# Performance work log

Measured on AMD Instinct MI355X. Metric: run time of the kernel, lower is better.

Reference implementation:

```python
import jax, jax.numpy as jnp
import numpy as np

NEG_SLOPE = 0.2  # PyG GATConv leaky_relu negative_slope
EPS = 1e-16      # PyG softmax denominator epsilon


def _add_self_loops(edge_index, edge_attr, N):
    # PyG add_self_loops with fill_value='mean': loop attr = mean of incoming edge attrs
    src, dst = edge_index[0], edge_index[1]
    ones = jnp.ones((src.shape[0],), edge_attr.dtype)
    cnt = jax.ops.segment_sum(ones, dst, num_segments=N)
    loop_attr = jax.ops.segment_sum(edge_attr, dst, num_segments=N) / jnp.maximum(cnt, 1.0)[:, None]
    loops = jnp.arange(N, dtype=src.dtype)
    return (jnp.concatenate([src, loops]),
            jnp.concatenate([dst, loops]),
            jnp.concatenate([edge_attr, loop_attr], axis=0))


def _gat_conv(x, src, dst, ea, W, We, att_src, att_dst, att_edge, bias, heads, out_ch):
    N = x.shape[0]
    h = (x @ W).reshape(N, heads, out_ch)              # [N,H,C]
    a_src = (h * att_src).sum(-1)                      # [N,H]
    a_dst = (h * att_dst).sum(-1)                      # [N,H]
    e = (ea @ We).reshape(-1, heads, out_ch)           # [E,H,C]
    a_edge = (e * att_edge).sum(-1)                    # [E,H]
    alpha = jax.nn.leaky_relu(a_src[src] + a_dst[dst] + a_edge, NEG_SLOPE)
    amax = jax.ops.segment_max(alpha, dst, num_segments=N)
    alpha = jnp.exp(alpha - amax[dst])
    denom = jax.ops.segment_sum(alpha, dst, num_segments=N)
    alpha = alpha / (denom[dst] + EPS)
    out = jax.ops.segment_sum(h[src] * alpha[..., None], dst, num_segments=N)  # [N,H,C]
    return out.mean(axis=1) + bias                     # concat=False -> mean over heads


def setup_inputs() -> dict:
    key = jax.random.key(0)
    ks = jax.random.split(key, 16)
    N, E, F_in, HID, OUT, H = 50000, 800000, 64, 16, 8, 8
    s = 0.1
    return {
        "x": jax.random.normal(ks[0], (N, F_in), jnp.float32),
        "edge_index": jax.random.randint(ks[1], (2, E), 0, N, dtype=jnp.int64),
        "edge_attr": jax.random.uniform(ks[2], (E, 1), jnp.float32),
        "W1": jax.random.normal(ks[3], (F_in, H * HID), jnp.float32) * s,
        "We1": jax.random.normal(ks[4], (1, H * HID), jnp.float32) * s,
        "att_src1": jax.random.normal(ks[5], (H, HID), jnp.float32) * s,
        "att_dst1": jax.random.normal(ks[6], (H, HID), jnp.float32) * s,
        "att_edge1": jax.random.normal(ks[7], (H, HID), jnp.float32) * s,
        "b1": jnp.zeros((HID,), jnp.float32),
        "W2": jax.random.normal(ks[8], (HID, OUT), jnp.float32) * s,
        "We2": jax.random.normal(ks[9], (1, OUT), jnp.float32) * s,
        "att_src2": jax.random.normal(ks[10], (1, OUT), jnp.float32) * s,
        "att_dst2": jax.random.normal(ks[11], (1, OUT), jnp.float32) * s,
        "att_edge2": jax.random.normal(ks[12], (1, OUT), jnp.float32) * s,
        "b2": jnp.zeros((OUT,), jnp.float32),
    }


def reference(x, edge_index, edge_attr, W1, We1, att_src1, att_dst1, att_edge1, b1,
              W2, We2, att_src2, att_dst2, att_edge2, b2):
    N = x.shape[0]
    src, dst, ea = _add_self_loops(edge_index, edge_attr, N)
    h = jax.nn.relu(_gat_conv(x, src, dst, ea, W1, We1, att_src1, att_dst1, att_edge1, b1, 8, 16))
    # dropout is identity in eval mode
    return _gat_conv(h, src, dst, ea, W2, We2, att_src2, att_dst2, att_edge2, b2, 1, 8)
```

## Files before the change

kernel.cpp:

```cpp
#include <hip/hip_runtime.h>
#include <hip/hip_fp16.h>
#include <math.h>

#define EPS 1e-16f
#define LOG2E 1.44269504088896340736f

typedef _Float16 half8 __attribute__((ext_vector_type(8)));
typedef float floatx4 __attribute__((ext_vector_type(4)));

#define RNG 4
#define NRR 16384
#define RB  64


__global__ __launch_bounds__(256) void k_hist(int E, int CH, const int* __restrict__ ei,
                                              int* __restrict__ H, int* __restrict__ rank) {
    int r = blockIdx.x / RB, b = blockIdx.x % RB;
    __shared__ int hist[NRR];
    for (int i = threadIdx.x; i < NRR; i += 256) hist[i] = 0;
    __syncthreads();
    int lo = b * CH, hi = min(E, (b + 1) * CH);
    int rlo = r << 14;
#pragma unroll 4
    for (int e = lo + threadIdx.x; e < hi; e += 256) {
        int d = ei[E + e];
        int dr = d - rlo;
        if ((unsigned)dr < NRR) rank[e] = atomicAdd(&hist[dr], 1);
    }
    __syncthreads();
    int* Hb = H + (size_t)blockIdx.x * NRR;
    for (int i = threadIdx.x; i < NRR; i += 256) Hb[i] = hist[i];
}

__global__ __launch_bounds__(256) void k_cntscan(int N, int* __restrict__ H,
                                                 int* rowptr, int* bsums) {
    __shared__ int sm[256];
    int t = threadIdx.x;
    int n = blockIdx.x * 256 + t;
    int sum = 0;
    if (n < N) {
        int r = n >> 14, dr = n & (NRR - 1);
        size_t base = ((size_t)(r * RB)) * NRR + dr;
#pragma unroll 8
        for (int b = 0; b < RB; ++b) {
            size_t idx = base + (size_t)b * NRR;
            int v = H[idx];
            H[idx] = sum;
            sum += v;
        }
    }
    int val = (n < N) ? (sum + 1) : 0;
    sm[t] = val; __syncthreads();
    for (int ofs = 1; ofs < 256; ofs <<= 1) {
        int v = (t >= ofs) ? sm[t - ofs] : 0;
        __syncthreads();
        sm[t] += v;
        __syncthreads();
    }
    if (n < N) rowptr[n] = sm[t] - val;
    if (t == 255) bsums[blockIdx.x] = sm[255];
}

__global__ void k_scan2(int nb, int N, int* bsums, int* rowptr) {
    __shared__ int sm[256];
    int t = threadIdx.x;
    int v = (t < nb) ? bsums[t] : 0;
    sm[t] = v; __syncthreads();
    for (int ofs = 1; ofs < 256; ofs <<= 1) {
        int u = (t >= ofs) ? sm[t - ofs] : 0;
        __syncthreads();
        sm[t] += u;
        __syncthreads();
    }
    if (t < nb) bsums[t] = sm[t] - v;
    if (t == 255) rowptr[N] = sm[255];
}

__global__ void k_scan3(int N, int* rowptr, const int* __restrict__ bsums) {
    int n = blockIdx.x * blockDim.x + threadIdx.x;
    if (n < N) rowptr[n] += bsums[n >> 8];
}

__global__ void k_scatter(int E, int CH, const int* __restrict__ ei, const float* __restrict__ ea,
                          const int* __restrict__ rowptr, const int* __restrict__ H,
                          const int* __restrict__ rank, int2* __restrict__ rec) {
    int e = blockIdx.x * blockDim.x + threadIdx.x;
    if (e >= E) return;
    int s = ei[e], d = ei[E + e];
    int r = d >> 14, dr = d & (NRR - 1);
    int b = e / CH;
    int pos = rowptr[d] + H[((size_t)(r * RB + b)) * NRR + dr] + rank[e];
    unsigned long long pk = ((unsigned long long)(unsigned)__float_as_int(ea[e]) << 32)
                          | (unsigned long long)(unsigned)s;
    __builtin_nontemporal_store(pk, (unsigned long long*)&rec[pos]);
}


__global__ __launch_bounds__(256) void k_misc(
    int N, int nbN, int Mpad, const int* __restrict__ rowptr, int2* __restrict__ rec,
    const float* __restrict__ x, _Float16* __restrict__ xh,
    const float* __restrict__ W1, _Float16* __restrict__ Wpk,
    const float* __restrict__ We1, const float* __restrict__ ae1,
    const float* __restrict__ We2, const float* __restrict__ ae2,
    float* __restrict__ wed) {
    int bid = blockIdx.x;
    if (bid < nbN) {
        int d = bid * 256 + threadIdx.x;
        if (d < N) {
            int start = rowptr[d], slot = rowptr[d + 1] - 1;
            float ssum = 0.0f;
            for (int i = start; i < slot; ++i) ssum += __int_as_float(rec[i].y);
            float mean = ssum / fmaxf((float)(slot - start), 1.0f);
            rec[slot] = make_int2(d, __float_as_int(mean));
        }
    } else if (bid < nbN + Mpad / 32) {
        int t = (bid - nbN) * 256 + threadIdx.x;
        int row = t >> 3;
        half8 h;
        if (row < N) {
            const float4* pp = (const float4*)(x + (size_t)t * 8);
            float4 f0 = pp[0], f1 = pp[1];
            h[0] = (_Float16)f0.x; h[1] = (_Float16)f0.y; h[2] = (_Float16)f0.z; h[3] = (_Float16)f0.w;
            h[4] = (_Float16)f1.x; h[5] = (_Float16)f1.y; h[6] = (_Float16)f1.z; h[7] = (_Float16)f1.w;
        } else {
#pragma unroll
            for (int i = 0; i < 8; ++i) h[i] = (_Float16)0.0f;
        }
        *(half8*)(xh + (size_t)t * 8) = h;
    } else {
        int t = threadIdx.x;
        for (int i = 0; i < 32; ++i) {
            int idx = i * 256 + t;
            int j  = idx & 7;
            int lq = (idx >> 3) & 63;
            int ks = (idx >> 9) & 1;
            int ct = idx >> 10;
            int k   = ks * 32 + (lq >> 4) * 8 + j;
            int col = ct * 16 + (lq & 15);
            Wpk[idx] = (_Float16)W1[k * 128 + col];
        }
        if (t < 8) {
            float ssum = 0.0f;
            for (int cc = 0; cc < 16; ++cc) ssum += We1[t * 16 + cc] * ae1[t * 16 + cc];
            wed[t] = ssum * LOG2E;
        }
        if (t == 8) {
            float ssum = 0.0f;
            for (int cc = 0; cc < 8; ++cc) ssum += We2[cc] * ae2[cc];
            wed[8] = ssum * LOG2E;
        }
    }
}


#define LDSP 132

__global__ __launch_bounds__(256) void k_gemm1m(
    int N, const _Float16* __restrict__ xh, const _Float16* __restrict__ Wpk,
    const float* __restrict__ att_s, const float* __restrict__ att_d,
    __half* __restrict__ h1, float* __restrict__ asrc, float* __restrict__ adst) {
    __shared__ float hs[4 * 16 * LDSP];
    int tid = threadIdx.x;
    int w = tid >> 6, l = tid & 63;
    int row0 = blockIdx.x * 64 + w * 16;
    int arow = row0 + (l & 15);
    half8 a0 = *(const half8*)(xh + (size_t)arow * 64 + (l >> 4) * 8);
    half8 a1 = *(const half8*)(xh + (size_t)arow * 64 + 32 + (l >> 4) * 8);
    float* base = &hs[w * 16 * LDSP];
    int r0 = (l >> 4) * 4;
#pragma unroll
    for (int ct = 0; ct < 8; ++ct) {
        half8 b0 = *(const half8*)(Wpk + ((ct * 2 + 0) * 64 + l) * 8);
        half8 b1 = *(const half8*)(Wpk + ((ct * 2 + 1) * 64 + l) * 8);
        floatx4 acc = {0.f, 0.f, 0.f, 0.f};
        acc = __builtin_amdgcn_mfma_f32_16x16x32_f16(a0, b0, acc, 0, 0, 0);
        acc = __builtin_amdgcn_mfma_f32_16x16x32_f16(a1, b1, acc, 0, 0, 0);
        int col = ct * 16 + (l & 15);
#pragma unroll
        for (int i = 0; i < 4; ++i)
            base[(r0 + i) * LDSP + col] = acc[i];
    }
    __syncthreads();
    int r = tid >> 2, g = tid & 3;
    int rg = blockIdx.x * 64 + r;
    if (rg >= N) return;
    float v[32];
    const float* rp = &hs[r * LDSP + g * 32];
#pragma unroll
    for (int j = 0; j < 8; ++j) {
        floatx4 t4 = *(const floatx4*)(rp + j * 4);
        v[j * 4 + 0] = t4[0]; v[j * 4 + 1] = t4[1];
        v[j * 4 + 2] = t4[2]; v[j * 4 + 3] = t4[3];
    }
    float vs0 = 0.f, vs1 = 0.f, vd0 = 0.f, vd1 = 0.f;
    const float4* as4 = (const float4*)(att_s + g * 32);
    const float4* ad4 = (const float4*)(att_d + g * 32);
#pragma unroll
    for (int j = 0; j < 4; ++j) {
        float4 a4 = as4[j], d4 = ad4[j];
        vs0 += v[j*4+0]*a4.x + v[j*4+1]*a4.y + v[j*4+2]*a4.z + v[j*4+3]*a4.w;
        vd0 += v[j*4+0]*d4.x + v[j*4+1]*d4.y + v[j*4+2]*d4.z + v[j*4+3]*d4.w;
    }
#pragma unroll
    for (int j = 4; j < 8; ++j) {
        float4 a4 = as4[j], d4 = ad4[j];
        vs1 += v[j*4+0]*a4.x + v[j*4+1]*a4.y + v[j*4+2]*a4.z + v[j*4+3]*a4.w;
        vd1 += v[j*4+0]*d4.x + v[j*4+1]*d4.y + v[j*4+2]*d4.z + v[j*4+3]*d4.w;
    }
    union { __half h[32]; float4 f4[4]; } u;
#pragma unroll
    for (int i = 0; i < 32; ++i) u.h[i] = __float2half(v[i]);
    float4* hp = (float4*)(h1 + (size_t)rg * 128 + g * 32);
#pragma unroll
    for (int j = 0; j < 4; ++j) hp[j] = u.f4[j];
    asrc[rg * 8 + g * 2]     = vs0 * LOG2E;
    asrc[rg * 8 + g * 2 + 1] = vs1 * LOG2E;
    adst[rg * 8 + g * 2]     = vd0 * LOG2E;
    adst[rg * 8 + g * 2 + 1] = vd1 * LOG2E;
}


__global__ __launch_bounds__(256) void k_agg1(
    int N, const int* __restrict__ rowptr, const int2* __restrict__ rec,
    const float* __restrict__ asrc1, const float* __restrict__ adst1,
    const float* __restrict__ wed,
    const __half* __restrict__ h1v, const float* __restrict__ b1,
    const float* __restrict__ W2, const float* __restrict__ as2w, const float* __restrict__ ad2w,
    float* __restrict__ hh2, float* __restrict__ asrc2, float* __restrict__ adst2) {
    __shared__ float hs[4 * 1040];
    int tid = threadIdx.x;
    int wid = (blockIdx.x * blockDim.x + tid) >> 6;
    if (wid >= N) return;
    int l = tid & 63, w = tid >> 6;
    int eo = l >> 3, hd = l & 7;
    int start = rowptr[wid], end = rowptr[wid + 1];
    int last = end - 1;
    int len = end - start;
    float adn = adst1[wid * 8 + hd];
    float wdh = wed[hd];
    const _Float16* h1p = (const _Float16*)h1v;

    float acc[16];
#pragma unroll
    for (int k = 0; k < 16; ++k) acc[k] = 0.f;
    float denom = 0.f;
    int e = start + eo;
    int2 rv  = rec[min(e, last)];
    int2 rn1 = rec[min(e + 8, last)];
    float av = asrc1[rv.x * 8 + hd];
    int nIt = (len + 7) >> 3;
    for (int it = 0; it < nIt; ++it) {
        const _Float16* hr = h1p + (((size_t)rv.x) << 7) + hd * 16;
        float4 hv0 = *(const float4*)hr;
        float4 hv1 = *(const float4*)(hr + 8);
        int2 rn2 = rec[min(e + 16, last)];
        float an = asrc1[rn1.x * 8 + hd];
        float a = av + adn + __int_as_float(rv.y) * wdh;
        a = fmaxf(a, 0.2f * a);
        float p = (e < end) ? exp2f(a) : 0.f;
        denom += p;
        const _Float16* x0 = (const _Float16*)&hv0;
        const _Float16* x1 = (const _Float16*)&hv1;
#pragma unroll
        for (int k = 0; k < 8; ++k) acc[k]     = fmaf(p, (float)x0[k], acc[k]);
#pragma unroll
        for (int k = 0; k < 8; ++k) acc[8 + k] = fmaf(p, (float)x1[k], acc[8 + k]);
        rv = rn1; rn1 = rn2; av = an; e += 8;
    }
    denom += __shfl_xor(denom, 8);
    denom += __shfl_xor(denom, 16);
    denom += __shfl_xor(denom, 32);
    float invd = 1.0f / (denom + EPS);
    float* hw = &hs[w * 1040];
#pragma unroll
    for (int k = 0; k < 16; ++k) hw[k * 65 + l] = acc[k] * invd;
    int c = l & 15, qt = l >> 4;
    const float* rp = &hw[c * 65 + qt * 16];
    float v = 0.f;
#pragma unroll
    for (int i = 0; i < 16; ++i) v += rp[i];
    v += __shfl_xor(v, 16);
    v += __shfl_xor(v, 32);
    float t = fmaxf(v * 0.125f + b1[c], 0.f);
    float p0 = t * W2[c * 8 + 2 * qt];
    float p1 = t * W2[c * 8 + 2 * qt + 1];
#pragma unroll
    for (int m = 1; m <= 8; m <<= 1) {
        p0 += __shfl_xor(p0, m);
        p1 += __shfl_xor(p1, m);
    }
    if (c == 0) *(float2*)&hh2[(size_t)wid * 8 + 2 * qt] = make_float2(p0, p1);
    float sd = p0 * as2w[2 * qt] + p1 * as2w[2 * qt + 1];
    float dd = p0 * ad2w[2 * qt] + p1 * ad2w[2 * qt + 1];
    sd += __shfl_xor(sd, 16); sd += __shfl_xor(sd, 32);
    dd += __shfl_xor(dd, 16); dd += __shfl_xor(dd, 32);
    if (l == 0) { asrc2[wid] = sd * LOG2E; adst2[wid] = dd * LOG2E; }
}


__global__ __launch_bounds__(256) void k_agg2(
    int N, const int* __restrict__ rowptr, const int2* __restrict__ rec,
    const float* __restrict__ asrc2, const float* __restrict__ adst2,
    const float* __restrict__ wed,
    const float* __restrict__ hh, const float* __restrict__ b2, float* __restrict__ out) {
    int wid = (blockIdx.x * blockDim.x + threadIdx.x) >> 6;
    if (wid >= N) return;
    int l = threadIdx.x & 63;
    int eo = l >> 3, c = l & 7;
    int start = rowptr[wid], end = rowptr[wid + 1];
    int len = end - start;
    int G = (len + 7) >> 3;
    int nIt = (G + 1) >> 1;
    int startB = start + (nIt << 3);
    int endA = min(startB, end);
    float adn = adst2[wid];
    float w2 = wed[8];

    float acc = 0.0f, denom = 0.0f;
    int eA = start + eo, eB = startB + eo;
    int last = end - 1;
    int2 rvA  = rec[min(eA, last)];
    int2 rnA1 = rec[min(eA + 8, last)];
    int2 rvB  = rec[min(eB, last)];
    int2 rnB1 = rec[min(eB + 8, last)];
    float avA = asrc2[rvA.x];
    float avB = asrc2[rvB.x];
    for (int it = 0; it < nIt; ++it) {
        float hvA = hh[(size_t)rvA.x * 8 + c];
        float hvB = hh[(size_t)rvB.x * 8 + c];
        int2 rnA2 = rec[min(eA + 16, last)];
        int2 rnB2 = rec[min(eB + 16, last)];
        float anA = asrc2[rnA1.x];
        float anB = asrc2[rnB1.x];
        float aA = avA + adn + __int_as_float(rvA.y) * w2;
        aA = fmaxf(aA, 0.2f * aA);
        float pA = (eA < endA) ? exp2f(aA) : 0.0f;
        float aB = avB + adn + __int_as_float(rvB.y) * w2;
        aB = fmaxf(aB, 0.2f * aB);
        float pB = (eB < end) ? exp2f(aB) : 0.0f;
        denom += pA + pB;
        acc = fmaf(pA, hvA, fmaf(pB, hvB, acc));
        rvA = rnA1; rnA1 = rnA2; avA = anA; eA += 8;
        rvB = rnB1; rnB1 = rnB2; avB = anB; eB += 8;
    }
    acc += __shfl_xor(acc, 8);  acc += __shfl_xor(acc, 16);  acc += __shfl_xor(acc, 32);
    denom += __shfl_xor(denom, 8); denom += __shfl_xor(denom, 16); denom += __shfl_xor(denom, 32);
    if (l < 8) out[(size_t)wid * 8 + l] = acc / (denom + EPS) + b2[l];
}


extern "C" void kernel_launch(void* const* d_in, const int* in_sizes, int n_in,
                              void* d_out, int out_size, void* d_ws, size_t ws_size,
                              hipStream_t stream) {
    const float* x        = (const float*)d_in[0];
    const int*   ei       = (const int*)d_in[1];
    const float* ea       = (const float*)d_in[2];
    const float* W1       = (const float*)d_in[3];
    const float* We1      = (const float*)d_in[4];
    const float* att_src1 = (const float*)d_in[5];
    const float* att_dst1 = (const float*)d_in[6];
    const float* att_edge1= (const float*)d_in[7];
    const float* b1       = (const float*)d_in[8];
    const float* W2       = (const float*)d_in[9];
    const float* We2      = (const float*)d_in[10];
    const float* att_src2 = (const float*)d_in[11];
    const float* att_dst2 = (const float*)d_in[12];
    const float* att_edge2= (const float*)d_in[13];
    const float* b2       = (const float*)d_in[14];
    float* out = (float*)d_out;

    const int N = in_sizes[0] / 64;
    const int E = in_sizes[2];
    const int E2 = E + N;
    const int CH = (E + RB - 1) / RB;
    const int NB64 = (N + 63) / 64;
    const int Mpad = NB64 * 64;

    char* p = (char*)d_ws;
    auto alloc = [&](size_t bytes) { void* r = (void*)p; p += (bytes + 255) & ~(size_t)255; return r; };
    int*   rowptr = (int*)  alloc((size_t)(N + 1) * 4);
    int*   bsums  = (int*)  alloc((size_t)4096 * 4);
    int2*  rec    = (int2*) alloc((size_t)E2 * 8);
    _Float16* Wpk = (_Float16*)alloc((size_t)8192 * 2);
    __half* h1    = (__half*)alloc((size_t)Mpad * 128 * 2);
    float* asrc1  = (float*)alloc((size_t)N * 8 * 4);
    float* adst1  = (float*)alloc((size_t)N * 8 * 4);
    float* hh2    = (float*)alloc((size_t)N * 8 * 4);
    float* asrc2  = (float*)alloc((size_t)N * 4);
    float* adst2  = (float*)alloc((size_t)N * 4);
    float* wed    = (float*)alloc(16 * 4);
    char* pS = p;
    int*   rank  = (int*)pS;
    int*   H     = (int*)(pS + (((size_t)E * 4 + 255) & ~(size_t)255));
    _Float16* xh = (_Float16*)pS;

    const int nbN = (N + 255) / 256;

    hipLaunchKernelGGL(k_hist,    dim3(RNG * RB), dim3(256), 0, stream, E, CH, ei, H, rank);
    hipLaunchKernelGGL(k_cntscan, dim3(nbN), dim3(256), 0, stream, N, H, rowptr, bsums);
    hipLaunchKernelGGL(k_scan2,   dim3(1), dim3(256), 0, stream, nbN, N, bsums, rowptr);
    hipLaunchKernelGGL(k_scan3,   dim3(nbN), dim3(256), 0, stream, N, rowptr, bsums);
    hipLaunchKernelGGL(k_scatter, dim3((E + 255) / 256), dim3(256), 0, stream, E, CH, ei, ea, rowptr, H, rank, rec);
    hipLaunchKernelGGL(k_misc,    dim3(nbN + Mpad / 32 + 1), dim3(256), 0, stream, N, nbN, Mpad, rowptr,
                       rec, x, xh, W1, Wpk, We1, att_edge1, We2, att_edge2, wed);
    hipLaunchKernelGGL(k_gemm1m,  dim3(NB64), dim3(256), 0, stream, N, xh, Wpk, att_src1, att_dst1, h1, asrc1, adst1);
    hipLaunchKernelGGL(k_agg1,    dim3((N + 3) / 4), dim3(256), 0, stream, N, rowptr, rec, asrc1, adst1, wed,
                       h1, b1, W2, att_src2, att_dst2, hh2, asrc2, adst2);
    hipLaunchKernelGGL(k_agg2,    dim3((N + 3) / 4), dim3(256), 0, stream, N, rowptr, rec, asrc2, adst2, wed,
                       hh2, b2, out);
}
```

Before: 143.7 us.

## Compute self-loops inline in aggregation and fuse edge scatter with layer-1 GEMM

Self-loop records are no longer stored in the CSR. Each aggregation kernel now sums the real edge weights per destination, derives the mean edge attribute, and adds the self-loop term directly from the node's own features. This removes the per-node pass in k_misc that computed and wrote the self-loop records, and shrinks the rec array. The edge scatter and the layer-1 MFMA GEMM are merged into one launch with a block-index split, which removes a kernel launch and lets both run concurrently. In exchange, xh, rank and H get separate workspace buffers instead of aliasing, and the aggregation kernels gain a reduction plus extra work on the first lane group.

```diff
diff --git a/kernel.cpp b/kernel.cpp
--- a/kernel.cpp
+++ b/kernel.cpp
@@ -49,7 +49,7 @@
             sum += v;
         }
     }
-    int val = (n < N) ? (sum + 1) : 0;
+    int val = (n < N) ? sum : 0;
     sm[t] = val; __syncthreads();
     for (int ofs = 1; ofs < 256; ofs <<= 1) {
         int v = (t >= ofs) ? sm[t - ofs] : 0;
@@ -81,40 +81,16 @@
     if (n < N) rowptr[n] += bsums[n >> 8];
 }
 
-__global__ void k_scatter(int E, int CH, const int* __restrict__ ei, const float* __restrict__ ea,
-                          const int* __restrict__ rowptr, const int* __restrict__ H,
-                          const int* __restrict__ rank, int2* __restrict__ rec) {
-    int e = blockIdx.x * blockDim.x + threadIdx.x;
-    if (e >= E) return;
-    int s = ei[e], d = ei[E + e];
-    int r = d >> 14, dr = d & (NRR - 1);
-    int b = e / CH;
-    int pos = rowptr[d] + H[((size_t)(r * RB + b)) * NRR + dr] + rank[e];
-    unsigned long long pk = ((unsigned long long)(unsigned)__float_as_int(ea[e]) << 32)
-                          | (unsigned long long)(unsigned)s;
-    __builtin_nontemporal_store(pk, (unsigned long long*)&rec[pos]);
-}
-
 
 __global__ __launch_bounds__(256) void k_misc(
-    int N, int nbN, int Mpad, const int* __restrict__ rowptr, int2* __restrict__ rec,
-    const float* __restrict__ x, _Float16* __restrict__ xh,
+    int N, int nbX, const float* __restrict__ x, _Float16* __restrict__ xh,
     const float* __restrict__ W1, _Float16* __restrict__ Wpk,
     const float* __restrict__ We1, const float* __restrict__ ae1,
     const float* __restrict__ We2, const float* __restrict__ ae2,
     float* __restrict__ wed) {
     int bid = blockIdx.x;
-    if (bid < nbN) {
-        int d = bid * 256 + threadIdx.x;
-        if (d < N) {
-            int start = rowptr[d], slot = rowptr[d + 1] - 1;
-            float ssum = 0.0f;
-            for (int i = start; i < slot; ++i) ssum += __int_as_float(rec[i].y);
-            float mean = ssum / fmaxf((float)(slot - start), 1.0f);
-            rec[slot] = make_int2(d, __float_as_int(mean));
-        }
-    } else if (bid < nbN + Mpad / 32) {
-        int t = (bid - nbN) * 256 + threadIdx.x;
+    if (bid < nbX) {
+        int t = bid * 256 + threadIdx.x;
         int row = t >> 3;
         half8 h;
         if (row < N) {
@@ -155,14 +131,30 @@
 
 #define LDSP 132
 
-__global__ __launch_bounds__(256) void k_gemm1m(
+__global__ __launch_bounds__(256) void k_scatgemm(
+    int E, int CH, int SB, const int* __restrict__ ei, const float* __restrict__ ea,
+    const int* __restrict__ rowptr, const int* __restrict__ H, const int* __restrict__ rank,
+    int2* __restrict__ rec,
     int N, const _Float16* __restrict__ xh, const _Float16* __restrict__ Wpk,
     const float* __restrict__ att_s, const float* __restrict__ att_d,
     __half* __restrict__ h1, float* __restrict__ asrc, float* __restrict__ adst) {
     __shared__ float hs[4 * 16 * LDSP];
+    if ((int)blockIdx.x < SB) {
+        int e = blockIdx.x * 256 + threadIdx.x;
+        if (e >= E) return;
+        int s = ei[e], d = ei[E + e];
+        int r = d >> 14, dr = d & (NRR - 1);
+        int b = e / CH;
+        int pos = rowptr[d] + H[((size_t)(r * RB + b)) * NRR + dr] + rank[e];
+        unsigned long long pk = ((unsigned long long)(unsigned)__float_as_int(ea[e]) << 32)
+                              | (unsigned long long)(unsigned)s;
+        __builtin_nontemporal_store(pk, (unsigned long long*)&rec[pos]);
+        return;
+    }
+    int blk = blockIdx.x - SB;
     int tid = threadIdx.x;
     int w = tid >> 6, l = tid & 63;
-    int row0 = blockIdx.x * 64 + w * 16;
+    int row0 = blk * 64 + w * 16;
     int arow = row0 + (l & 15);
     half8 a0 = *(const half8*)(xh + (size_t)arow * 64 + (l >> 4) * 8);
     half8 a1 = *(const half8*)(xh + (size_t)arow * 64 + 32 + (l >> 4) * 8);
@@ -182,7 +174,7 @@
     }
     __syncthreads();
     int r = tid >> 2, g = tid & 3;
-    int rg = blockIdx.x * 64 + r;
+    int rg = blk * 64 + r;
     if (rg >= N) return;
     float v[32];
     const float* rp = &hs[r * LDSP + g * 32];
@@ -234,8 +226,9 @@
     int l = tid & 63, w = tid >> 6;
     int eo = l >> 3, hd = l & 7;
     int start = rowptr[wid], end = rowptr[wid + 1];
+    int len = end - start;
     int last = end - 1;
-    int len = end - start;
+    bool has = (len > 0);
     float adn = adst1[wid * 8 + hd];
     float wdh = wed[hd];
     const _Float16* h1p = (const _Float16*)h1v;
@@ -243,10 +236,10 @@
     float acc[16];
 #pragma unroll
     for (int k = 0; k < 16; ++k) acc[k] = 0.f;
-    float denom = 0.f;
+    float denom = 0.f, esum = 0.f;
     int e = start + eo;
-    int2 rv  = rec[min(e, last)];
-    int2 rn1 = rec[min(e + 8, last)];
+    int2 rv  = rec[has ? min(e, last) : 0];
+    int2 rn1 = rec[has ? min(e + 8, last) : 0];
     float av = asrc1[rv.x * 8 + hd];
     int nIt = (len + 7) >> 3;
     for (int it = 0; it < nIt; ++it) {
@@ -255,9 +248,12 @@
         float4 hv1 = *(const float4*)(hr + 8);
         int2 rn2 = rec[min(e + 16, last)];
         float an = asrc1[rn1.x * 8 + hd];
-        float a = av + adn + __int_as_float(rv.y) * wdh;
+        float wgt = __int_as_float(rv.y);
+        float a = av + adn + wgt * wdh;
         a = fmaxf(a, 0.2f * a);
-        float p = (e < end) ? exp2f(a) : 0.f;
+        bool valid = (e < end);
+        float p = valid ? exp2f(a) : 0.f;
+        esum += valid ? wgt : 0.f;
         denom += p;
         const _Float16* x0 = (const _Float16*)&hv0;
         const _Float16* x1 = (const _Float16*)&hv1;
@@ -266,6 +262,25 @@
 #pragma unroll
         for (int k = 0; k < 8; ++k) acc[8 + k] = fmaf(p, (float)x1[k], acc[8 + k]);
         rv = rn1; rn1 = rn2; av = an; e += 8;
+    }
+    esum += __shfl_xor(esum, 8);
+    esum += __shfl_xor(esum, 16);
+    esum += __shfl_xor(esum, 32);
+    float mean = esum / (float)max(len, 1);
+    float aself = asrc1[wid * 8 + hd] + adn + mean * wdh;
+    aself = fmaxf(aself, 0.2f * aself);
+    float pself = exp2f(aself);
+    if (eo == 0) {
+        denom += pself;
+        const _Float16* hr = h1p + (((size_t)wid) << 7) + hd * 16;
+        float4 hv0 = *(const float4*)hr;
+        float4 hv1 = *(const float4*)(hr + 8);
+        const _Float16* x0 = (const _Float16*)&hv0;
+        const _Float16* x1 = (const _Float16*)&hv1;
+#pragma unroll
+        for (int k = 0; k < 8; ++k) acc[k]     = fmaf(pself, (float)x0[k], acc[k]);
+#pragma unroll
+        for (int k = 0; k < 8; ++k) acc[8 + k] = fmaf(pself, (float)x1[k], acc[8 + k]);
     }
     denom += __shfl_xor(denom, 8);
     denom += __shfl_xor(denom, 16);
@@ -309,6 +324,8 @@
     int eo = l >> 3, c = l & 7;
     int start = rowptr[wid], end = rowptr[wid + 1];
     int len = end - start;
+    int last = end - 1;
+    bool has = (len > 0);
     int G = (len + 7) >> 3;
     int nIt = (G + 1) >> 1;
     int startB = start + (nIt << 3);
@@ -316,13 +333,12 @@
     float adn = adst2[wid];
     float w2 = wed[8];
 
-    float acc = 0.0f, denom = 0.0f;
+    float acc = 0.0f, denom = 0.0f, esum = 0.0f;
     int eA = start + eo, eB = startB + eo;
-    int last = end - 1;
-    int2 rvA  = rec[min(eA, last)];
-    int2 rnA1 = rec[min(eA + 8, last)];
-    int2 rvB  = rec[min(eB, last)];
-    int2 rnB1 = rec[min(eB + 8, last)];
+    int2 rvA  = rec[has ? min(eA, last) : 0];
+    int2 rnA1 = rec[has ? min(eA + 8, last) : 0];
+    int2 rvB  = rec[has ? min(eB, last) : 0];
+    int2 rnB1 = rec[has ? min(eB + 8, last) : 0];
     float avA = asrc2[rvA.x];
     float avB = asrc2[rvB.x];
     for (int it = 0; it < nIt; ++it) {
@@ -332,16 +348,30 @@
         int2 rnB2 = rec[min(eB + 16, last)];
         float anA = asrc2[rnA1.x];
         float anB = asrc2[rnB1.x];
-        float aA = avA + adn + __int_as_float(rvA.y) * w2;
+        float wA = __int_as_float(rvA.y);
+        float wB = __int_as_float(rvB.y);
+        float aA = avA + adn + wA * w2;
         aA = fmaxf(aA, 0.2f * aA);
-        float pA = (eA < endA) ? exp2f(aA) : 0.0f;
-        float aB = avB + adn + __int_as_float(rvB.y) * w2;
+        bool vA = (eA < endA);
+        float pA = vA ? exp2f(aA) : 0.0f;
+        float aB = avB + adn + wB * w2;
         aB = fmaxf(aB, 0.2f * aB);
-        float pB = (eB < end) ? exp2f(aB) : 0.0f;
+        bool vB = (eB < end);
+        float pB = vB ? exp2f(aB) : 0.0f;
+        esum += (vA ? wA : 0.f) + (vB ? wB : 0.f);
         denom += pA + pB;
         acc = fmaf(pA, hvA, fmaf(pB, hvB, acc));
         rvA = rnA1; rnA1 = rnA2; avA = anA; eA += 8;
         rvB = rnB1; rnB1 = rnB2; avB = anB; eB += 8;
+    }
+    esum += __shfl_xor(esum, 8); esum += __shfl_xor(esum, 16); esum += __shfl_xor(esum, 32);
+    float mean = esum / (float)max(len, 1);
+    float aself = asrc2[wid] + adn + mean * w2;
+    aself = fmaxf(aself, 0.2f * aself);
+    float pself = exp2f(aself);
+    if (eo == 0) {
+        denom += pself;
+        acc = fmaf(pself, hh[(size_t)wid * 8 + c], acc);
     }
     acc += __shfl_xor(acc, 8);  acc += __shfl_xor(acc, 16);  acc += __shfl_xor(acc, 32);
     denom += __shfl_xor(denom, 8); denom += __shfl_xor(denom, 16); denom += __shfl_xor(denom, 32);
@@ -371,17 +401,18 @@
 
     const int N = in_sizes[0] / 64;
     const int E = in_sizes[2];
-    const int E2 = E + N;
     const int CH = (E + RB - 1) / RB;
     const int NB64 = (N + 63) / 64;
     const int Mpad = NB64 * 64;
+    const int SB = (E + 255) / 256;
 
     char* p = (char*)d_ws;
     auto alloc = [&](size_t bytes) { void* r = (void*)p; p += (bytes + 255) & ~(size_t)255; return r; };
     int*   rowptr = (int*)  alloc((size_t)(N + 1) * 4);
     int*   bsums  = (int*)  alloc((size_t)4096 * 4);
-    int2*  rec    = (int2*) alloc((size_t)E2 * 8);
+    int2*  rec    = (int2*) alloc((size_t)E * 8);
     _Float16* Wpk = (_Float16*)alloc((size_t)8192 * 2);
+    _Float16* xh  = (_Float16*)alloc((size_t)Mpad * 64 * 2);
     __half* h1    = (__half*)alloc((size_t)Mpad * 128 * 2);
     float* asrc1  = (float*)alloc((size_t)N * 8 * 4);
     float* adst1  = (float*)alloc((size_t)N * 8 * 4);
@@ -389,23 +420,22 @@
     float* asrc2  = (float*)alloc((size_t)N * 4);
     float* adst2  = (float*)alloc((size_t)N * 4);
     float* wed    = (float*)alloc(16 * 4);
-    char* pS = p;
-    int*   rank  = (int*)pS;
-    int*   H     = (int*)(pS + (((size_t)E * 4 + 255) & ~(size_t)255));
-    _Float16* xh = (_Float16*)pS;
+    int*   rank   = (int*)  alloc((size_t)E * 4);
+    int*   H      = (int*)  alloc((size_t)RNG * RB * NRR * 4);
 
     const int nbN = (N + 255) / 256;
-
-    hipLaunchKernelGGL(k_hist,    dim3(RNG * RB), dim3(256), 0, stream, E, CH, ei, H, rank);
-    hipLaunchKernelGGL(k_cntscan, dim3(nbN), dim3(256), 0, stream, N, H, rowptr, bsums);
-    hipLaunchKernelGGL(k_scan2,   dim3(1), dim3(256), 0, stream, nbN, N, bsums, rowptr);
-    hipLaunchKernelGGL(k_scan3,   dim3(nbN), dim3(256), 0, stream, N, rowptr, bsums);
-    hipLaunchKernelGGL(k_scatter, dim3((E + 255) / 256), dim3(256), 0, stream, E, CH, ei, ea, rowptr, H, rank, rec);
-    hipLaunchKernelGGL(k_misc,    dim3(nbN + Mpad / 32 + 1), dim3(256), 0, stream, N, nbN, Mpad, rowptr,
-                       rec, x, xh, W1, Wpk, We1, att_edge1, We2, att_edge2, wed);
-    hipLaunchKernelGGL(k_gemm1m,  dim3(NB64), dim3(256), 0, stream, N, xh, Wpk, att_src1, att_dst1, h1, asrc1, adst1);
-    hipLaunchKernelGGL(k_agg1,    dim3((N + 3) / 4), dim3(256), 0, stream, N, rowptr, rec, asrc1, adst1, wed,
-                       h1, b1, W2, att_src2, att_dst2, hh2, asrc2, adst2);
-    hipLaunchKernelGGL(k_agg2,    dim3((N + 3) / 4), dim3(256), 0, stream, N, rowptr, rec, asrc2, adst2, wed,
-                       hh2, b2, out);
-}
+    const int nbX = Mpad / 32;
+
+    hipLaunchKernelGGL(k_misc,     dim3(nbX + 1), dim3(256), 0, stream, N, nbX,
+                       x, xh, W1, Wpk, We1, att_edge1, We2, att_edge2, wed);
+    hipLaunchKernelGGL(k_hist,     dim3(RNG * RB), dim3(256), 0, stream, E, CH, ei, H, rank);
+    hipLaunchKernelGGL(k_cntscan,  dim3(nbN), dim3(256), 0, stream, N, H, rowptr, bsums);
+    hipLaunchKernelGGL(k_scan2,    dim3(1), dim3(256), 0, stream, nbN, N, bsums, rowptr);
+    hipLaunchKernelGGL(k_scan3,    dim3(nbN), dim3(256), 0, stream, N, rowptr, bsums);
+    hipLaunchKernelGGL(k_scatgemm, dim3(SB + NB64), dim3(256), 0, stream, E, CH, SB, ei, ea,
+                       rowptr, H, rank, rec, N, xh, Wpk, att_src1, att_dst1, h1, asrc1, adst1);
+    hipLaunchKernelGGL(k_agg1,     dim3((N + 3) / 4), dim3(256), 0, stream, N, rowptr, rec,
+                       asrc1, adst1, wed, h1, b1, W2, att_src2, att_dst2, hh2, asrc2, adst2);
+    hipLaunchKernelGGL(k_agg2,     dim3((N + 3) / 4), dim3(256), 0, stream, N, rowptr, rec,
+                       asrc2, adst2, wed, hh2, b2, out);
+}
```

After: 138.5 us. 1.04x faster.
